# Kernel optimization log

Hardware: AMD Instinct MI355X
Metric: run time of the kernel (lower is better)

Reference implementation:

```python
import jax, jax.numpy as jnp
import numpy as np

N_USER, N_ITEM, D = 50000, 30000, 64
N = N_USER + N_ITEM
NNZ_UI, NNZ_R, NNZ_II = 1000000, 800000, 300000
IMG_F, TXT_F = 512, 384
EPS = 1e-5


def spmm(rows, cols, vals, x, n_out):
    # sparse [n_out, n_in] @ dense [n_in, d] via gather + segment-sum
    return jax.ops.segment_sum(vals[:, None] * x[cols], rows, num_segments=n_out)


def leaky_relu(x):
    return jnp.where(x >= 0, x, 0.01 * x)


def setup_inputs() -> dict:
    key = jax.random.key(0)
    ks = jax.random.split(key, 32)
    f = lambda i, shape, s=0.05: (jax.random.normal(ks[i], shape, dtype=jnp.float32) * s)
    inp = {
        'user_emb': f(0, (N_USER, D)),
        'item_emb': f(1, (N_ITEM, D)),
        'image_embedding': f(2, (N_ITEM, IMG_F), 1.0),
        'text_embedding': f(3, (N_ITEM, TXT_F), 1.0),
        'W_img': f(4, (IMG_F, D)), 'b_img': jnp.zeros((D,), jnp.float32),
        'bn_g_img': jnp.ones((D,), jnp.float32), 'bn_b_img': jnp.zeros((D,), jnp.float32),
        'W_txt': f(5, (TXT_F, D)), 'b_txt': jnp.zeros((D,), jnp.float32),
        'bn_g_txt': jnp.ones((D,), jnp.float32), 'bn_b_txt': jnp.zeros((D,), jnp.float32),
        'W_gate_img': f(6, (D, D)), 'b_gate_img': jnp.zeros((D,), jnp.float32),
        'W_gate_txt': f(7, (D, D)), 'b_gate_txt': jnp.zeros((D,), jnp.float32),
        'W_common1': f(8, (D, D)), 'b_common1': jnp.zeros((D,), jnp.float32),
        'w_common2': f(9, (D,)),
        'ui_vals': jax.random.uniform(ks[10], (NNZ_UI,), dtype=jnp.float32),
        'R_vals': jax.random.uniform(ks[11], (NNZ_R,), dtype=jnp.float32),
        'ii_img_vals': jax.random.uniform(ks[12], (NNZ_II,), dtype=jnp.float32),
        'ii_txt_vals': jax.random.uniform(ks[13], (NNZ_II,), dtype=jnp.float32),
        'ui_rows': jax.random.randint(ks[14], (NNZ_UI,), 0, N, dtype=jnp.int32),
        'ui_cols': jax.random.randint(ks[15], (NNZ_UI,), 0, N, dtype=jnp.int32),
        'R_rows': jax.random.randint(ks[16], (NNZ_R,), 0, N_USER, dtype=jnp.int32),
        'R_cols': jax.random.randint(ks[17], (NNZ_R,), 0, N_ITEM, dtype=jnp.int32),
        'ii_img_rows': jax.random.randint(ks[18], (NNZ_II,), 0, N_ITEM, dtype=jnp.int32),
        'ii_img_cols': jax.random.randint(ks[19], (NNZ_II,), 0, N_ITEM, dtype=jnp.int32),
        'ii_txt_rows': jax.random.randint(ks[20], (NNZ_II,), 0, N_ITEM, dtype=jnp.int32),
        'ii_txt_cols': jax.random.randint(ks[21], (NNZ_II,), 0, N_ITEM, dtype=jnp.int32),
    }
    return inp


def reference(user_emb, item_emb, image_embedding, text_embedding,
              W_img, b_img, bn_g_img, bn_b_img,
              W_txt, b_txt, bn_g_txt, bn_b_txt,
              W_gate_img, b_gate_img, W_gate_txt, b_gate_txt,
              W_common1, b_common1, w_common2,
              ui_vals, R_vals, ii_img_vals, ii_txt_vals,
              ui_rows, ui_cols, R_rows, R_cols,
              ii_img_rows, ii_img_cols, ii_txt_rows, ii_txt_cols):
    # ---- user_item_GCN: adj = original + diffusion (fused edge list) ----
    cat = jnp.concatenate([item_emb, user_emb], axis=0)  # [N, D], item first per source
    embs = [cat]
    for _ in range(2):
        cat = spmm(ui_rows, ui_cols, ui_vals, cat, N)
        embs.append(cat)
    content_embedding = jnp.stack(embs, axis=1).mean(axis=1)  # [N, D]

    # ---- modal projections (BN inference, dropout=eval identity) ----
    def project(x, W, b, g, beta):
        h = x @ W + b
        h = h * (g / jnp.sqrt(1.0 + EPS)) + beta  # BatchNorm1d, running stats (0, 1)
        return leaky_relu(h)

    img_feat = project(image_embedding, W_img, b_img, bn_g_img, bn_b_img)  # [I, D]
    txt_feat = project(text_embedding, W_txt, b_txt, bn_g_txt, bn_b_txt)

    # ---- item_item_GCN ----
    def modal_branch(feat, Wg, bg, rows, cols, vals):
        it = item_emb * jax.nn.sigmoid(feat @ Wg + bg)  # gated item embedding
        for _ in range(2):
            it = spmm(rows, cols, vals, it, N_ITEM)
        us = spmm(R_rows, R_cols, R_vals, it, N_USER)  # R @ item -> user
        return jnp.concatenate([us, it], axis=0)  # [N, D], user first per source

    image_ui = modal_branch(img_feat, W_gate_img, b_gate_img, ii_img_rows, ii_img_cols, ii_img_vals)
    text_ui = modal_branch(txt_feat, W_gate_txt, b_gate_txt, ii_txt_rows, ii_txt_cols, ii_txt_vals)

    # ---- gate_attention_fusion (non-tiktok: 2 modalities) ----
    def att_score(e):
        return leaky_relu(e @ W_common1 + b_common1) @ w_common2  # [N]

    att = jnp.stack([att_score(image_ui), att_score(text_ui)], axis=-1)  # [N, 2]
    w = jax.nn.softmax(att, axis=-1)
    common = w[:, 0:1] * image_ui + w[:, 1:2] * text_ui
    special_img = image_ui - common
    special_txt = text_ui - common

    return jnp.stack([content_embedding, special_img, special_txt, common], axis=0)  # [4, N, D]
```

## Files before the change

### kernel.cpp

```cpp
#include <hip/hip_runtime.h>

#define N_USER 50000
#define N_ITEM 30000
#define DIM    64
#define NTOT   80000
#define NNZ_UI 1000000
#define NNZ_R  800000
#define NNZ_II 300000
#define IMG_F  512
#define TXT_F  384

#define NROWS_ALL 190000
#define NNZ_ALL   2400000
#define BASE_R    NTOT
#define BASE_II   (NTOT + N_USER)
#define BASE_IT   (NTOT + N_USER + N_ITEM)

#define RB_BITS   9
#define RB_ROWS   512
#define NBUCK     ((NROWS_ALL + RB_ROWS - 1) / RB_ROWS)
#define NBLK_A2   400
#define EDG_A2    6000

__device__ __forceinline__ int edge_row(int i,
        const int* __restrict__ r0, const int* __restrict__ r1,
        const int* __restrict__ r2, const int* __restrict__ r3){
    if (i < NNZ_UI)                       return r0[i];
    if (i < NNZ_UI + NNZ_R)               return BASE_R  + r1[i - NNZ_UI];
    if (i < NNZ_UI + NNZ_R + NNZ_II)      return BASE_II + r2[i - NNZ_UI - NNZ_R];
    return BASE_IT + r3[i - NNZ_UI - NNZ_R - NNZ_II];
}

__device__ __forceinline__ void edge_all(int i,
        const int* __restrict__ r0, const int* __restrict__ c0, const float* __restrict__ v0,
        const int* __restrict__ r1, const int* __restrict__ c1, const float* __restrict__ v1,
        const int* __restrict__ r2, const int* __restrict__ c2, const float* __restrict__ v2,
        const int* __restrict__ r3, const int* __restrict__ c3, const float* __restrict__ v3,
        int& gr, int& col, float& val){
    if (i < NNZ_UI){
        gr = r0[i]; col = c0[i]; val = v0[i];
    } else if (i < NNZ_UI + NNZ_R){
        int j = i - NNZ_UI;               gr = BASE_R  + r1[j]; col = c1[j]; val = v1[j];
    } else if (i < NNZ_UI + NNZ_R + NNZ_II){
        int j = i - NNZ_UI - NNZ_R;       gr = BASE_II + r2[j]; col = c2[j]; val = v2[j];
    } else {
        int j = i - NNZ_UI - NNZ_R - NNZ_II; gr = BASE_IT + r3[j]; col = c3[j]; val = v3[j];
    }
}

__global__ __launch_bounds__(256) void k_bhist(const int* __restrict__ r0,
        const int* __restrict__ r1, const int* __restrict__ r2,
        const int* __restrict__ r3, int* __restrict__ bcnt){
    __shared__ int h[NBUCK];
    for (int i = threadIdx.x; i < NBUCK; i += 256) h[i] = 0;
    __syncthreads();
    const int stride = gridDim.x * 256;
    for (int i = blockIdx.x * 256 + threadIdx.x; i < NNZ_ALL; i += stride){
        int gr = edge_row(i, r0, r1, r2, r3);
        atomicAdd(&h[gr >> RB_BITS], 1);
    }
    __syncthreads();
    for (int i = threadIdx.x; i < NBUCK; i += 256){
        int c = h[i];
        if (c) atomicAdd(&bcnt[i], c);
    }
}

__global__ __launch_bounds__(512) void k_bscan(const int* __restrict__ bcnt,
        int* __restrict__ bbase, int* __restrict__ off){
    __shared__ int sh[512];
    const int t = threadIdx.x;
    int v = (t < NBUCK) ? bcnt[t] : 0;
    sh[t] = v;
    __syncthreads();
    for (int d = 1; d < 512; d <<= 1){
        int u = (t >= d) ? sh[t - d] : 0;
        __syncthreads();
        sh[t] += u;
        __syncthreads();
    }
    if (t < NBUCK) bbase[t] = sh[t] - v;
    if (t == NBUCK - 1){
        bbase[NBUCK] = sh[t];
        off[NROWS_ALL] = sh[t];
    }
}

__global__ __launch_bounds__(256) void k_bin(
        const int* __restrict__ r0, const int* __restrict__ c0, const float* __restrict__ v0,
        const int* __restrict__ r1, const int* __restrict__ c1, const float* __restrict__ v1,
        const int* __restrict__ r2, const int* __restrict__ c2, const float* __restrict__ v2,
        const int* __restrict__ r3, const int* __restrict__ c3, const float* __restrict__ v3,
        const int* __restrict__ bbase, int* __restrict__ bcur,
        int2* __restrict__ binned){
    __shared__ int lofs[NBUCK];
    __shared__ int lcur[NBUCK];
    const int t = threadIdx.x;
    for (int i = t; i < NBUCK; i += 256){ lofs[i] = 0; lcur[i] = 0; }
    __syncthreads();
    const int s0 = blockIdx.x * EDG_A2, s1 = s0 + EDG_A2;
    for (int i = s0 + t; i < s1; i += 256){
        int gr = edge_row(i, r0, r1, r2, r3);
        atomicAdd(&lofs[gr >> RB_BITS], 1);
    }
    __syncthreads();
    for (int i = t; i < NBUCK; i += 256){
        int c = lofs[i];
        lofs[i] = c ? (bbase[i] + atomicAdd(&bcur[i], c)) : 0;
    }
    __syncthreads();
    for (int i = s0 + t; i < s1; i += 256){
        int gr, col; float val;
        edge_all(i, r0, c0, v0, r1, c1, v1, r2, c2, v2, r3, c3, v3, gr, col, val);
        int b = gr >> RB_BITS;
        int slot = atomicAdd(&lcur[b], 1);
        binned[lofs[b] + slot] = make_int2((col << RB_BITS) | (gr & (RB_ROWS - 1)),
                                           __float_as_int(val));
    }
}

__global__ __launch_bounds__(256) void k_scatter(const int* __restrict__ bbase,
        const int2* __restrict__ binned, int* __restrict__ off,
        int2* __restrict__ csr){
    __shared__ int h[RB_ROWS];
    const int t = threadIdx.x;
    const int b = blockIdx.x;
    const int base = bbase[b];
    const int nb = bbase[b + 1] - base;
    h[t] = 0; h[t + 256] = 0;
    __syncthreads();
    for (int i = t; i < nb; i += 256)
        atomicAdd(&h[binned[base + i].x & (RB_ROWS - 1)], 1);
    __syncthreads();
    if (t < 64){
        int v[8], s = 0;
#pragma unroll
        for (int k = 0; k < 8; ++k){ v[k] = h[t * 8 + k]; s += v[k]; }
        int incl = s;
#pragma unroll
        for (int d = 1; d < 64; d <<= 1){
            int u = __shfl_up(incl, d, 64);
            if (t >= d) incl += u;
        }
        int run = incl - s;
#pragma unroll
        for (int k = 0; k < 8; ++k){ int tmp = v[k]; h[t * 8 + k] = run; run += tmp; }
    }
    __syncthreads();
    const int row0 = b << RB_BITS;
    for (int i = t; i < RB_ROWS; i += 256){
        int r = row0 + i;
        if (r < NROWS_ALL) off[r] = base + h[i];
    }
    __syncthreads();
    for (int i = t; i < nb; i += 256){
        int2 rec = binned[base + i];
        int lr = rec.x & (RB_ROWS - 1);
        int slot = atomicAdd(&h[lr], 1);
        csr[base + slot] = make_int2(rec.x >> RB_BITS, rec.y);
    }
}

__global__ void k_cat0(const float* __restrict__ item, const float* __restrict__ user,
                       float* __restrict__ o1){
    int i = blockIdx.x * 256 + threadIdx.x;
    const int ITEMS = N_ITEM * DIM;
    o1[i] = (i < ITEMS) ? item[i] : user[i - ITEMS];
}

__global__ void k_pull(const int* __restrict__ off, const int2* __restrict__ csr,
                       const float* __restrict__ x, float* __restrict__ y, int nrows){
    int t = blockIdx.x * 256 + threadIdx.x;
    int r = t >> 4;
    if (r >= nrows) return;
    int l = (t & 15) << 2;
    int s = off[r], e = off[r + 1];
    float4 a0 = {0.f, 0.f, 0.f, 0.f};
    float4 a1 = {0.f, 0.f, 0.f, 0.f};
    int j = s;
    for (; j + 2 <= e; j += 2){
        int2 e0 = csr[j];
        int2 e1 = csr[j + 1];
        float v0 = __int_as_float(e0.y);
        float v1 = __int_as_float(e1.y);
        const float4 x0 = *reinterpret_cast<const float4*>(x + ((long)e0.x << 6) + l);
        const float4 x1 = *reinterpret_cast<const float4*>(x + ((long)e1.x << 6) + l);
        a0.x = fmaf(v0, x0.x, a0.x);
        a0.y = fmaf(v0, x0.y, a0.y);
        a0.z = fmaf(v0, x0.z, a0.z);
        a0.w = fmaf(v0, x0.w, a0.w);
        a1.x = fmaf(v1, x1.x, a1.x);
        a1.y = fmaf(v1, x1.y, a1.y);
        a1.z = fmaf(v1, x1.z, a1.z);
        a1.w = fmaf(v1, x1.w, a1.w);
    }
    if (j < e){
        int2 e0 = csr[j];
        float v0 = __int_as_float(e0.y);
        const float4 x0 = *reinterpret_cast<const float4*>(x + ((long)e0.x << 6) + l);
        a0.x = fmaf(v0, x0.x, a0.x);
        a0.y = fmaf(v0, x0.y, a0.y);
        a0.z = fmaf(v0, x0.z, a0.z);
        a0.w = fmaf(v0, x0.w, a0.w);
    }
    a0.x += a1.x; a0.y += a1.y; a0.z += a1.z; a0.w += a1.w;
    *reinterpret_cast<float4*>(y + ((long)r << 6) + l) = a0;
}

__global__ void k_pull_mean(const int* __restrict__ off, const int2* __restrict__ csr,
                            const float* __restrict__ x, const float* __restrict__ a,
                            float* __restrict__ o0, int nrows){
    int t = blockIdx.x * 256 + threadIdx.x;
    int r = t >> 4;
    if (r >= nrows) return;
    int l = (t & 15) << 2;
    int s = off[r], e = off[r + 1];
    float4 a0 = {0.f, 0.f, 0.f, 0.f};
    float4 a1 = {0.f, 0.f, 0.f, 0.f};
    int j = s;
    for (; j + 2 <= e; j += 2){
        int2 e0 = csr[j];
        int2 e1 = csr[j + 1];
        float v0 = __int_as_float(e0.y);
        float v1 = __int_as_float(e1.y);
        const float4 x0 = *reinterpret_cast<const float4*>(x + ((long)e0.x << 6) + l);
        const float4 x1 = *reinterpret_cast<const float4*>(x + ((long)e1.x << 6) + l);
        a0.x = fmaf(v0, x0.x, a0.x);
        a0.y = fmaf(v0, x0.y, a0.y);
        a0.z = fmaf(v0, x0.z, a0.z);
        a0.w = fmaf(v0, x0.w, a0.w);
        a1.x = fmaf(v1, x1.x, a1.x);
        a1.y = fmaf(v1, x1.y, a1.y);
        a1.z = fmaf(v1, x1.z, a1.z);
        a1.w = fmaf(v1, x1.w, a1.w);
    }
    if (j < e){
        int2 e0 = csr[j];
        float v0 = __int_as_float(e0.y);
        const float4 x0 = *reinterpret_cast<const float4*>(x + ((long)e0.x << 6) + l);
        a0.x = fmaf(v0, x0.x, a0.x);
        a0.y = fmaf(v0, x0.y, a0.y);
        a0.z = fmaf(v0, x0.z, a0.z);
        a0.w = fmaf(v0, x0.w, a0.w);
    }
    const float4 av = *reinterpret_cast<const float4*>(a + ((long)r << 6) + l);
    const float4 xv = *reinterpret_cast<const float4*>(x + ((long)r << 6) + l);
    float4 o;
    o.x = (av.x + xv.x + a0.x + a1.x) * (1.0f / 3.0f);
    o.y = (av.y + xv.y + a0.y + a1.y) * (1.0f / 3.0f);
    o.z = (av.z + xv.z + a0.z + a1.z) * (1.0f / 3.0f);
    o.w = (av.w + xv.w + a0.w + a1.w) * (1.0f / 3.0f);
    *reinterpret_cast<float4*>(o0 + ((long)r << 6) + l) = o;
}

template<int K>
__global__ __launch_bounds__(256) void k_projgate(
        const float* __restrict__ X,
        const float* __restrict__ W,  const float* __restrict__ b,
        const float* __restrict__ g,  const float* __restrict__ beta,
        const float* __restrict__ Wg, const float* __restrict__ bg,
        const float* __restrict__ item, float* __restrict__ outP){
    __shared__ float xs[48][68];
    __shared__ float ws[64][64];
    const int t  = threadIdx.x;
    const int tr = t >> 4;
    const int tc = t & 15;
    const int row0 = blockIdx.x * 48;

    float acc[3][4];
#pragma unroll
    for (int i = 0; i < 3; ++i)
#pragma unroll
        for (int j = 0; j < 4; ++j) acc[i][j] = 0.f;

    for (int ks = 0; ks < K; ks += 64){
        __syncthreads();
#pragma unroll
        for (int i = 0; i < 3; ++i){
            int r = tr + 16 * i;
            *reinterpret_cast<float4*>(&xs[r][tc * 4]) =
                *reinterpret_cast<const float4*>(X + (long)(row0 + r) * K + ks + tc * 4);
        }
        {
            const float4* wsrc = reinterpret_cast<const float4*>(W + (long)ks * 64);
            float4* wdst = reinterpret_cast<float4*>(&ws[0][0]);
#pragma unroll
            for (int i = 0; i < 4; ++i) wdst[t + 256 * i] = wsrc[t + 256 * i];
        }
        __syncthreads();
#pragma unroll 8
        for (int kk = 0; kk < 64; kk += 2){
            float2 a[3];
#pragma unroll
            for (int i = 0; i < 3; ++i)
                a[i] = *reinterpret_cast<const float2*>(&xs[tr + 16 * i][kk]);
            float4 b0 = *reinterpret_cast<const float4*>(&ws[kk][tc * 4]);
            float4 b1 = *reinterpret_cast<const float4*>(&ws[kk + 1][tc * 4]);
#pragma unroll
            for (int i = 0; i < 3; ++i){
                acc[i][0] = fmaf(a[i].x, b0.x, acc[i][0]);
                acc[i][1] = fmaf(a[i].x, b0.y, acc[i][1]);
                acc[i][2] = fmaf(a[i].x, b0.z, acc[i][2]);
                acc[i][3] = fmaf(a[i].x, b0.w, acc[i][3]);
                acc[i][0] = fmaf(a[i].y, b1.x, acc[i][0]);
                acc[i][1] = fmaf(a[i].y, b1.y, acc[i][1]);
                acc[i][2] = fmaf(a[i].y, b1.z, acc[i][2]);
                acc[i][3] = fmaf(a[i].y, b1.w, acc[i][3]);
            }
        }
    }

    const float4 b4  = reinterpret_cast<const float4*>(b)[tc];
    const float4 g4  = reinterpret_cast<const float4*>(g)[tc];
    const float4 be4 = reinterpret_cast<const float4*>(beta)[tc];
    __syncthreads();
#pragma unroll
    for (int i = 0; i < 3; ++i){
        int r = tr + 16 * i;
        float4 h;
        h.x = (acc[i][0] + b4.x) * (g4.x * 0.99999500003749943f) + be4.x;
        h.y = (acc[i][1] + b4.y) * (g4.y * 0.99999500003749943f) + be4.y;
        h.z = (acc[i][2] + b4.z) * (g4.z * 0.99999500003749943f) + be4.z;
        h.w = (acc[i][3] + b4.w) * (g4.w * 0.99999500003749943f) + be4.w;
        h.x = (h.x >= 0.f) ? h.x : 0.01f * h.x;
        h.y = (h.y >= 0.f) ? h.y : 0.01f * h.y;
        h.z = (h.z >= 0.f) ? h.z : 0.01f * h.z;
        h.w = (h.w >= 0.f) ? h.w : 0.01f * h.w;
        *reinterpret_cast<float4*>(&xs[r][tc * 4]) = h;
    }
    {
        const float4* wsrc = reinterpret_cast<const float4*>(Wg);
        float4* wdst = reinterpret_cast<float4*>(&ws[0][0]);
#pragma unroll
        for (int i = 0; i < 4; ++i) wdst[t + 256 * i] = wsrc[t + 256 * i];
    }
    __syncthreads();

    float ac2[3][4];
#pragma unroll
    for (int i = 0; i < 3; ++i)
#pragma unroll
        for (int j = 0; j < 4; ++j) ac2[i][j] = 0.f;
#pragma unroll 8
    for (int kk = 0; kk < 64; kk += 2){
        float2 a[3];
#pragma unroll
        for (int i = 0; i < 3; ++i)
            a[i] = *reinterpret_cast<const float2*>(&xs[tr + 16 * i][kk]);
        float4 b0 = *reinterpret_cast<const float4*>(&ws[kk][tc * 4]);
        float4 b1 = *reinterpret_cast<const float4*>(&ws[kk + 1][tc * 4]);
#pragma unroll
        for (int i = 0; i < 3; ++i){
            ac2[i][0] = fmaf(a[i].x, b0.x, ac2[i][0]);
            ac2[i][1] = fmaf(a[i].x, b0.y, ac2[i][1]);
            ac2[i][2] = fmaf(a[i].x, b0.z, ac2[i][2]);
            ac2[i][3] = fmaf(a[i].x, b0.w, ac2[i][3]);
            ac2[i][0] = fmaf(a[i].y, b1.x, ac2[i][0]);
            ac2[i][1] = fmaf(a[i].y, b1.y, ac2[i][1]);
            ac2[i][2] = fmaf(a[i].y, b1.z, ac2[i][2]);
            ac2[i][3] = fmaf(a[i].y, b1.w, ac2[i][3]);
        }
    }

    const float4 bg4 = reinterpret_cast<const float4*>(bg)[tc];
#pragma unroll
    for (int i = 0; i < 3; ++i){
        int r = tr + 16 * i;
        const float4 iv = *reinterpret_cast<const float4*>(
                item + (long)(row0 + r) * 64 + tc * 4);
        float4 o;
        o.x = iv.x / (1.f + __expf(-(ac2[i][0] + bg4.x)));
        o.y = iv.y / (1.f + __expf(-(ac2[i][1] + bg4.y)));
        o.z = iv.z / (1.f + __expf(-(ac2[i][2] + bg4.z)));
        o.w = iv.w / (1.f + __expf(-(ac2[i][3] + bg4.w)));
        *reinterpret_cast<float4*>(outP + (long)(row0 + r) * 64 + tc * 4) = o;
    }
}

__global__ __launch_bounds__(256) void k_fuse(const float* __restrict__ img,
        const float* __restrict__ txt, const float* __restrict__ W1,
        const float* __restrict__ b1, const float* __restrict__ w2,
        float* __restrict__ out){
    __shared__ float si[64][68];
    __shared__ float st[64][68];
    __shared__ float w1s[64][64];
    const int t  = threadIdx.x;
    const int tr = t >> 4;
    const int tc = t & 15;
    const long row0 = (long)blockIdx.x * 64;

#pragma unroll
    for (int i = 0; i < 4; ++i){
        int r = tr + 16 * i;
        *reinterpret_cast<float4*>(&si[r][tc * 4]) =
            *reinterpret_cast<const float4*>(img + (row0 + r) * 64 + tc * 4);
        *reinterpret_cast<float4*>(&st[r][tc * 4]) =
            *reinterpret_cast<const float4*>(txt + (row0 + r) * 64 + tc * 4);
    }
    {
        const float4* wsrc = reinterpret_cast<const float4*>(W1);
        float4* wdst = reinterpret_cast<float4*>(&w1s[0][0]);
#pragma unroll
        for (int i = 0; i < 4; ++i) wdst[t + 256 * i] = wsrc[t + 256 * i];
    }
    __syncthreads();

    float ai[4][4], at[4][4];
#pragma unroll
    for (int i = 0; i < 4; ++i)
#pragma unroll
        for (int j = 0; j < 4; ++j){ ai[i][j] = 0.f; at[i][j] = 0.f; }

#pragma unroll 8
    for (int kk = 0; kk < 64; kk += 2){
        float4 b0 = *reinterpret_cast<const float4*>(&w1s[kk][tc * 4]);
        float4 b1v = *reinterpret_cast<const float4*>(&w1s[kk + 1][tc * 4]);
#pragma unroll
        for (int i = 0; i < 4; ++i){
            float2 a = *reinterpret_cast<const float2*>(&si[tr + 16 * i][kk]);
            float2 c = *reinterpret_cast<const float2*>(&st[tr + 16 * i][kk]);
            ai[i][0] = fmaf(a.x, b0.x, ai[i][0]);
            ai[i][1] = fmaf(a.x, b0.y, ai[i][1]);
            ai[i][2] = fmaf(a.x, b0.z, ai[i][2]);
            ai[i][3] = fmaf(a.x, b0.w, ai[i][3]);
            ai[i][0] = fmaf(a.y, b1v.x, ai[i][0]);
            ai[i][1] = fmaf(a.y, b1v.y, ai[i][1]);
            ai[i][2] = fmaf(a.y, b1v.z, ai[i][2]);
            ai[i][3] = fmaf(a.y, b1v.w, ai[i][3]);
            at[i][0] = fmaf(c.x, b0.x, at[i][0]);
            at[i][1] = fmaf(c.x, b0.y, at[i][1]);
            at[i][2] = fmaf(c.x, b0.z, at[i][2]);
            at[i][3] = fmaf(c.x, b0.w, at[i][3]);
            at[i][0] = fmaf(c.y, b1v.x, at[i][0]);
            at[i][1] = fmaf(c.y, b1v.y, at[i][1]);
            at[i][2] = fmaf(c.y, b1v.z, at[i][2]);
            at[i][3] = fmaf(c.y, b1v.w, at[i][3]);
        }
    }

    const float4 b14 = reinterpret_cast<const float4*>(b1)[tc];
    const float4 w24 = reinterpret_cast<const float4*>(w2)[tc];
    float pi[4], pt[4];
#pragma unroll
    for (int i = 0; i < 4; ++i){
        float hi0 = ai[i][0] + b14.x; hi0 = (hi0 >= 0.f) ? hi0 : 0.01f * hi0;
        float hi1 = ai[i][1] + b14.y; hi1 = (hi1 >= 0.f) ? hi1 : 0.01f * hi1;
        float hi2 = ai[i][2] + b14.z; hi2 = (hi2 >= 0.f) ? hi2 : 0.01f * hi2;
        float hi3 = ai[i][3] + b14.w; hi3 = (hi3 >= 0.f) ? hi3 : 0.01f * hi3;
        float ht0 = at[i][0] + b14.x; ht0 = (ht0 >= 0.f) ? ht0 : 0.01f * ht0;
        float ht1 = at[i][1] + b14.y; ht1 = (ht1 >= 0.f) ? ht1 : 0.01f * ht1;
        float ht2 = at[i][2] + b14.z; ht2 = (ht2 >= 0.f) ? ht2 : 0.01f * ht2;
        float ht3 = at[i][3] + b14.w; ht3 = (ht3 >= 0.f) ? ht3 : 0.01f * ht3;
        pi[i] = fmaf(hi0, w24.x, fmaf(hi1, w24.y, fmaf(hi2, w24.z, hi3 * w24.w)));
        pt[i] = fmaf(ht0, w24.x, fmaf(ht1, w24.y, fmaf(ht2, w24.z, ht3 * w24.w)));
    }
#pragma unroll
    for (int m = 1; m < 16; m <<= 1){
#pragma unroll
        for (int i = 0; i < 4; ++i){
            pi[i] += __shfl_xor(pi[i], m, 64);
            pt[i] += __shfl_xor(pt[i], m, 64);
        }
    }

    const long NTD = (long)NTOT * DIM;
#pragma unroll
    for (int i = 0; i < 4; ++i){
        int r = tr + 16 * i;
        float mx = fmaxf(pi[i], pt[i]);
        float ei = __expf(pi[i] - mx), et = __expf(pt[i] - mx);
        float inv = 1.f / (ei + et);
        float wi = ei * inv, wt = et * inv;
        const float4 ie = *reinterpret_cast<const float4*>(&si[r][tc * 4]);
        const float4 te = *reinterpret_cast<const float4*>(&st[r][tc * 4]);
        float4 cm, oi, ot;
        cm.x = wi * ie.x + wt * te.x;
        cm.y = wi * ie.y + wt * te.y;
        cm.z = wi * ie.z + wt * te.z;
        cm.w = wi * ie.w + wt * te.w;
        oi.x = ie.x - cm.x; oi.y = ie.y - cm.y; oi.z = ie.z - cm.z; oi.w = ie.w - cm.w;
        ot.x = te.x - cm.x; ot.y = te.y - cm.y; ot.z = te.z - cm.z; ot.w = te.w - cm.w;
        long o = (row0 + r) * 64 + tc * 4;
        *reinterpret_cast<float4*>(out + NTD + o)     = oi;
        *reinterpret_cast<float4*>(out + 2 * NTD + o) = ot;
        *reinterpret_cast<float4*>(out + 3 * NTD + o) = cm;
    }
}

extern "C" void kernel_launch(void* const* d_in, const int* in_sizes, int n_in,
                              void* d_out, int out_size, void* d_ws, size_t ws_size,
                              hipStream_t stream){
    const float* user_emb  = (const float*)d_in[0];
    const float* item_emb  = (const float*)d_in[1];
    const float* image_emb = (const float*)d_in[2];
    const float* text_emb  = (const float*)d_in[3];
    const float* W_img = (const float*)d_in[4];
    const float* b_img = (const float*)d_in[5];
    const float* g_img = (const float*)d_in[6];
    const float* be_img= (const float*)d_in[7];
    const float* W_txt = (const float*)d_in[8];
    const float* b_txt = (const float*)d_in[9];
    const float* g_txt = (const float*)d_in[10];
    const float* be_txt= (const float*)d_in[11];
    const float* W_gi  = (const float*)d_in[12];
    const float* b_gi  = (const float*)d_in[13];
    const float* W_gt  = (const float*)d_in[14];
    const float* b_gt  = (const float*)d_in[15];
    const float* W_c1  = (const float*)d_in[16];
    const float* b_c1  = (const float*)d_in[17];
    const float* w_c2  = (const float*)d_in[18];
    const float* ui_vals = (const float*)d_in[19];
    const float* R_vals  = (const float*)d_in[20];
    const float* ii_iv   = (const float*)d_in[21];
    const float* ii_tv   = (const float*)d_in[22];
    const int* ui_rows = (const int*)d_in[23];
    const int* ui_cols = (const int*)d_in[24];
    const int* R_rows  = (const int*)d_in[25];
    const int* R_cols  = (const int*)d_in[26];
    const int* ii_ir   = (const int*)d_in[27];
    const int* ii_ic   = (const int*)d_in[28];
    const int* ii_tr   = (const int*)d_in[29];
    const int* ii_tc   = (const int*)d_in[30];

    const long ND = (long)NTOT * DIM;
    const long ID = (long)N_ITEM * DIM;
    const long UD = (long)N_USER * DIM;

    float* out = (float*)d_out;
    float* o0 = out;
    float* o1 = out + ND;
    float* o2 = out + 2 * ND;
    float* o3 = out + 3 * ND;

    float* P = o3;
    float* Q = o3 + ID;

    int2* binned = (int2*)o0;

    int2* csr   = (int2*)d_ws;
    int*  off   = (int*)(csr + NNZ_ALL);
    int*  bcnt  = off + NROWS_ALL + 4;
    int*  bcur  = bcnt + NBUCK;
    int*  bbase = bcur + NBUCK;

    hipMemsetAsync(bcnt, 0, 2 * NBUCK * sizeof(int), stream);
    k_bhist<<<512, 256, 0, stream>>>(ui_rows, R_rows, ii_ir, ii_tr, bcnt);
    k_bscan<<<1, 512, 0, stream>>>(bcnt, bbase, off);
    k_bin<<<NBLK_A2, 256, 0, stream>>>(
        ui_rows, ui_cols, ui_vals,  R_rows, R_cols, R_vals,
        ii_ir, ii_ic, ii_iv,        ii_tr, ii_tc, ii_tv,
        bbase, bcur, binned);
    k_scatter<<<NBUCK, 256, 0, stream>>>(bbase, binned, off, csr);

    const int* offUI = off;
    const int* offR  = off + BASE_R;
    const int* offI2 = off + BASE_II;
    const int* offT2 = off + BASE_IT;

    k_cat0<<<ND / 256, 256, 0, stream>>>(item_emb, user_emb, o1);
    k_pull<<<NTOT / 16, 256, 0, stream>>>(offUI, csr, o1, o2, NTOT);
    k_pull_mean<<<NTOT / 16, 256, 0, stream>>>(offUI, csr, o2, o1, o0, NTOT);

    k_projgate<IMG_F><<<N_ITEM / 48, 256, 0, stream>>>(
        image_emb, W_img, b_img, g_img, be_img, W_gi, b_gi, item_emb, P);
    k_pull<<<N_ITEM / 16, 256, 0, stream>>>(offI2, csr, P, Q, N_ITEM);
    k_pull<<<N_ITEM / 16, 256, 0, stream>>>(offI2, csr, Q, o1 + UD, N_ITEM);
    k_pull<<<N_USER / 16, 256, 0, stream>>>(offR, csr, o1 + UD, o1, N_USER);

    k_projgate<TXT_F><<<N_ITEM / 48, 256, 0, stream>>>(
        text_emb, W_txt, b_txt, g_txt, be_txt, W_gt, b_gt, item_emb, P);
    k_pull<<<N_ITEM / 16, 256, 0, stream>>>(offT2, csr, P, Q, N_ITEM);
    k_pull<<<N_ITEM / 16, 256, 0, stream>>>(offT2, csr, Q, o2 + UD, N_ITEM);
    k_pull<<<N_USER / 16, 256, 0, stream>>>(offR, csr, o2 + UD, o2, N_USER);

    k_fuse<<<NTOT / 64, 256, 0, stream>>>(o1, o2, W_c1, b_c1, w_c2, out);
}
```

Before: 592.5 us.

## Batch image and text branches into joint launches and double-buffer projection GEMM

The image and text modal branches now share launches. One projection-plus-gate kernel covers both modalities by block index, and a two-way pull kernel runs each SpMM step for both branches at once. This roughly halves the branch launches and gives each launch twice as many independent blocks to fill the GPU. The projection GEMM also prefetches the next K chunk into registers while computing on a double-buffered shared tile, and reads four K values per LDS load. The cost is doubled shared memory per block, which may lower occupancy, and intermediate buffers reassigned into output slices o1 and o2 that must not overlap.

```diff
diff --git a/kernel.cpp b/kernel.cpp
--- a/kernel.cpp
+++ b/kernel.cpp
@@ -21,6 +21,10 @@
 #define NBUCK     ((NROWS_ALL + RB_ROWS - 1) / RB_ROWS)
 #define NBLK_A2   400
 #define EDG_A2    6000
+
+#define NBLK_PG   625
+#define NBLK_I16  1875
+#define NBLK_U16  3125
 
 __device__ __forceinline__ int edge_row(int i,
         const int* __restrict__ r0, const int* __restrict__ r1,
@@ -168,12 +172,9 @@
     o1[i] = (i < ITEMS) ? item[i] : user[i - ITEMS];
 }
 
-__global__ void k_pull(const int* __restrict__ off, const int2* __restrict__ csr,
-                       const float* __restrict__ x, float* __restrict__ y, int nrows){
-    int t = blockIdx.x * 256 + threadIdx.x;
-    int r = t >> 4;
-    if (r >= nrows) return;
-    int l = (t & 15) << 2;
+__device__ __forceinline__ void pull_body(const int* __restrict__ off,
+        const int2* __restrict__ csr, const float* __restrict__ x,
+        float* __restrict__ y, int r, int l){
     int s = off[r], e = off[r + 1];
     float4 a0 = {0.f, 0.f, 0.f, 0.f};
     float4 a1 = {0.f, 0.f, 0.f, 0.f};
@@ -205,6 +206,28 @@
     }
     a0.x += a1.x; a0.y += a1.y; a0.z += a1.z; a0.w += a1.w;
     *reinterpret_cast<float4*>(y + ((long)r << 6) + l) = a0;
+}
+
+__global__ void k_pull(const int* __restrict__ off, const int2* __restrict__ csr,
+                       const float* __restrict__ x, float* __restrict__ y, int nrows){
+    int t = blockIdx.x * 256 + threadIdx.x;
+    int r = t >> 4;
+    if (r >= nrows) return;
+    pull_body(off, csr, x, y, r, (t & 15) << 2);
+}
+
+__global__ void k_pull2(const int* __restrict__ offA, const int2* __restrict__ csr,
+                        const float* __restrict__ xA, float* __restrict__ yA,
+                        const int* __restrict__ offB, const float* __restrict__ xB,
+                        float* __restrict__ yB, int nrows, int nblk_half){
+    int b = blockIdx.x;
+    const int* off; const float* x; float* y;
+    if (b < nblk_half){ off = offA; x = xA; y = yA; }
+    else              { b -= nblk_half; off = offB; x = xB; y = yB; }
+    int t = b * 256 + threadIdx.x;
+    int r = t >> 4;
+    if (r >= nrows) return;
+    pull_body(off, csr, x, y, r, (t & 15) << 2);
 }
 
 __global__ void k_pull_mean(const int* __restrict__ off, const int2* __restrict__ csr,
@@ -253,19 +276,56 @@
     *reinterpret_cast<float4*>(o0 + ((long)r << 6) + l) = o;
 }
 
-template<int K>
-__global__ __launch_bounds__(256) void k_projgate(
-        const float* __restrict__ X,
-        const float* __restrict__ W,  const float* __restrict__ b,
-        const float* __restrict__ g,  const float* __restrict__ beta,
-        const float* __restrict__ Wg, const float* __restrict__ bg,
-        const float* __restrict__ item, float* __restrict__ outP){
-    __shared__ float xs[48][68];
-    __shared__ float ws[64][64];
+__global__ __launch_bounds__(256) void k_projgate2(
+        const float* __restrict__ Xi, const float* __restrict__ Wi,
+        const float* __restrict__ bi, const float* __restrict__ gi,
+        const float* __restrict__ bei, const float* __restrict__ Wgi,
+        const float* __restrict__ bgi,
+        const float* __restrict__ Xt, const float* __restrict__ Wt,
+        const float* __restrict__ bt, const float* __restrict__ gt,
+        const float* __restrict__ bet, const float* __restrict__ Wgt,
+        const float* __restrict__ bgt,
+        const float* __restrict__ item,
+        float* __restrict__ Pi, float* __restrict__ Pt){
+    __shared__ float xs[2][48][68];
+    __shared__ float ws[2][64][64];
     const int t  = threadIdx.x;
     const int tr = t >> 4;
     const int tc = t & 15;
-    const int row0 = blockIdx.x * 48;
+
+    const bool isTxt = blockIdx.x >= NBLK_PG;
+    const int  blk   = isTxt ? (blockIdx.x - NBLK_PG) : blockIdx.x;
+    const int  K     = isTxt ? TXT_F : IMG_F;
+    const int  NC    = K >> 6;
+    const float* X   = isTxt ? Xt  : Xi;
+    const float* W   = isTxt ? Wt  : Wi;
+    const float* bb  = isTxt ? bt  : bi;
+    const float* gg  = isTxt ? gt  : gi;
+    const float* be  = isTxt ? bet : bei;
+    const float* Wg  = isTxt ? Wgt : Wgi;
+    const float* bg  = isTxt ? bgt : bgi;
+    float* outP      = isTxt ? Pt  : Pi;
+    const int row0   = blk * 48;
+
+    float4 px[3], pw[4];
+#pragma unroll
+    for (int i = 0; i < 3; ++i)
+        px[i] = *reinterpret_cast<const float4*>(
+                X + (long)(row0 + tr + 16 * i) * K + tc * 4);
+    {
+        const float4* wsrc = reinterpret_cast<const float4*>(W);
+#pragma unroll
+        for (int i = 0; i < 4; ++i) pw[i] = wsrc[t + 256 * i];
+    }
+#pragma unroll
+    for (int i = 0; i < 3; ++i)
+        *reinterpret_cast<float4*>(&xs[0][tr + 16 * i][tc * 4]) = px[i];
+    {
+        float4* wdst = reinterpret_cast<float4*>(&ws[0][0][0]);
+#pragma unroll
+        for (int i = 0; i < 4; ++i) wdst[t + 256 * i] = pw[i];
+    }
+    __syncthreads();
 
     float acc[3][4];
 #pragma unroll
@@ -273,47 +333,64 @@
 #pragma unroll
         for (int j = 0; j < 4; ++j) acc[i][j] = 0.f;
 
-    for (int ks = 0; ks < K; ks += 64){
-        __syncthreads();
-#pragma unroll
-        for (int i = 0; i < 3; ++i){
-            int r = tr + 16 * i;
-            *reinterpret_cast<float4*>(&xs[r][tc * 4]) =
-                *reinterpret_cast<const float4*>(X + (long)(row0 + r) * K + ks + tc * 4);
+    for (int c = 0; c < NC; ++c){
+        const int cur = c & 1;
+        const bool has_next = (c + 1 < NC);
+        if (has_next){
+#pragma unroll
+            for (int i = 0; i < 3; ++i)
+                px[i] = *reinterpret_cast<const float4*>(
+                        X + (long)(row0 + tr + 16 * i) * K + (c + 1) * 64 + tc * 4);
+            const float4* wsrc = reinterpret_cast<const float4*>(W + (long)(c + 1) * 64 * 64);
+#pragma unroll
+            for (int i = 0; i < 4; ++i) pw[i] = wsrc[t + 256 * i];
         }
-        {
-            const float4* wsrc = reinterpret_cast<const float4*>(W + (long)ks * 64);
-            float4* wdst = reinterpret_cast<float4*>(&ws[0][0]);
-#pragma unroll
-            for (int i = 0; i < 4; ++i) wdst[t + 256 * i] = wsrc[t + 256 * i];
-        }
-        __syncthreads();
-#pragma unroll 8
-        for (int kk = 0; kk < 64; kk += 2){
-            float2 a[3];
+#pragma unroll 4
+        for (int kk = 0; kk < 64; kk += 4){
+            float4 a[3];
 #pragma unroll
             for (int i = 0; i < 3; ++i)
-                a[i] = *reinterpret_cast<const float2*>(&xs[tr + 16 * i][kk]);
-            float4 b0 = *reinterpret_cast<const float4*>(&ws[kk][tc * 4]);
-            float4 b1 = *reinterpret_cast<const float4*>(&ws[kk + 1][tc * 4]);
+                a[i] = *reinterpret_cast<const float4*>(&xs[cur][tr + 16 * i][kk]);
+            float4 w0 = *reinterpret_cast<const float4*>(&ws[cur][kk][tc * 4]);
+            float4 w1 = *reinterpret_cast<const float4*>(&ws[cur][kk + 1][tc * 4]);
+            float4 w2 = *reinterpret_cast<const float4*>(&ws[cur][kk + 2][tc * 4]);
+            float4 w3 = *reinterpret_cast<const float4*>(&ws[cur][kk + 3][tc * 4]);
 #pragma unroll
             for (int i = 0; i < 3; ++i){
-                acc[i][0] = fmaf(a[i].x, b0.x, acc[i][0]);
-                acc[i][1] = fmaf(a[i].x, b0.y, acc[i][1]);
-                acc[i][2] = fmaf(a[i].x, b0.z, acc[i][2]);
-                acc[i][3] = fmaf(a[i].x, b0.w, acc[i][3]);
-                acc[i][0] = fmaf(a[i].y, b1.x, acc[i][0]);
-                acc[i][1] = fmaf(a[i].y, b1.y, acc[i][1]);
-                acc[i][2] = fmaf(a[i].y, b1.z, acc[i][2]);
-                acc[i][3] = fmaf(a[i].y, b1.w, acc[i][3]);
+                acc[i][0] = fmaf(a[i].x, w0.x, acc[i][0]);
+                acc[i][1] = fmaf(a[i].x, w0.y, acc[i][1]);
+                acc[i][2] = fmaf(a[i].x, w0.z, acc[i][2]);
+                acc[i][3] = fmaf(a[i].x, w0.w, acc[i][3]);
+                acc[i][0] = fmaf(a[i].y, w1.x, acc[i][0]);
+                acc[i][1] = fmaf(a[i].y, w1.y, acc[i][1]);
+                acc[i][2] = fmaf(a[i].y, w1.z, acc[i][2]);
+                acc[i][3] = fmaf(a[i].y, w1.w, acc[i][3]);
+                acc[i][0] = fmaf(a[i].z, w2.x, acc[i][0]);
+                acc[i][1] = fmaf(a[i].z, w2.y, acc[i][1]);
+                acc[i][2] = fmaf(a[i].z, w2.z, acc[i][2]);
+                acc[i][3] = fmaf(a[i].z, w2.w, acc[i][3]);
+                acc[i][0] = fmaf(a[i].w, w3.x, acc[i][0]);
+                acc[i][1] = fmaf(a[i].w, w3.y, acc[i][1]);
+                acc[i][2] = fmaf(a[i].w, w3.z, acc[i][2]);
+                acc[i][3] = fmaf(a[i].w, w3.w, acc[i][3]);
             }
         }
-    }
-
-    const float4 b4  = reinterpret_cast<const float4*>(b)[tc];
-    const float4 g4  = reinterpret_cast<const float4*>(g)[tc];
-    const float4 be4 = reinterpret_cast<const float4*>(beta)[tc];
-    __syncthreads();
+        if (has_next){
+            const int nxt = cur ^ 1;
+#pragma unroll
+            for (int i = 0; i < 3; ++i)
+                *reinterpret_cast<float4*>(&xs[nxt][tr + 16 * i][tc * 4]) = px[i];
+            float4* wdst = reinterpret_cast<float4*>(&ws[nxt][0][0]);
+#pragma unroll
+            for (int i = 0; i < 4; ++i) wdst[t + 256 * i] = pw[i];
+            __syncthreads();
+        }
+    }
+    __syncthreads();
+
+    const float4 b4  = reinterpret_cast<const float4*>(bb)[tc];
+    const float4 g4  = reinterpret_cast<const float4*>(gg)[tc];
+    const float4 be4 = reinterpret_cast<const float4*>(be)[tc];
 #pragma unroll
     for (int i = 0; i < 3; ++i){
         int r = tr + 16 * i;
@@ -326,39 +403,48 @@
         h.y = (h.y >= 0.f) ? h.y : 0.01f * h.y;
         h.z = (h.z >= 0.f) ? h.z : 0.01f * h.z;
         h.w = (h.w >= 0.f) ? h.w : 0.01f * h.w;
-        *reinterpret_cast<float4*>(&xs[r][tc * 4]) = h;
+        *reinterpret_cast<float4*>(&xs[0][r][tc * 4]) = h;
     }
     {
         const float4* wsrc = reinterpret_cast<const float4*>(Wg);
-        float4* wdst = reinterpret_cast<float4*>(&ws[0][0]);
+        float4* wdst = reinterpret_cast<float4*>(&ws[0][0][0]);
 #pragma unroll
         for (int i = 0; i < 4; ++i) wdst[t + 256 * i] = wsrc[t + 256 * i];
     }
     __syncthreads();
 
-    float ac2[3][4];
 #pragma unroll
     for (int i = 0; i < 3; ++i)
 #pragma unroll
-        for (int j = 0; j < 4; ++j) ac2[i][j] = 0.f;
-#pragma unroll 8
-    for (int kk = 0; kk < 64; kk += 2){
-        float2 a[3];
+        for (int j = 0; j < 4; ++j) acc[i][j] = 0.f;
+#pragma unroll 4
+    for (int kk = 0; kk < 64; kk += 4){
+        float4 a[3];
 #pragma unroll
         for (int i = 0; i < 3; ++i)
-            a[i] = *reinterpret_cast<const float2*>(&xs[tr + 16 * i][kk]);
-        float4 b0 = *reinterpret_cast<const float4*>(&ws[kk][tc * 4]);
-        float4 b1 = *reinterpret_cast<const float4*>(&ws[kk + 1][tc * 4]);
+            a[i] = *reinterpret_cast<const float4*>(&xs[0][tr + 16 * i][kk]);
+        float4 w0 = *reinterpret_cast<const float4*>(&ws[0][kk][tc * 4]);
+        float4 w1 = *reinterpret_cast<const float4*>(&ws[0][kk + 1][tc * 4]);
+        float4 w2 = *reinterpret_cast<const float4*>(&ws[0][kk + 2][tc * 4]);
+        float4 w3 = *reinterpret_cast<const float4*>(&ws[0][kk + 3][tc * 4]);
 #pragma unroll
         for (int i = 0; i < 3; ++i){
-            ac2[i][0] = fmaf(a[i].x, b0.x, ac2[i][0]);
-            ac2[i][1] = fmaf(a[i].x, b0.y, ac2[i][1]);
-            ac2[i][2] = fmaf(a[i].x, b0.z, ac2[i][2]);
-            ac2[i][3] = fmaf(a[i].x, b0.w, ac2[i][3]);
-            ac2[i][0] = fmaf(a[i].y, b1.x, ac2[i][0]);
-            ac2[i][1] = fmaf(a[i].y, b1.y, ac2[i][1]);
-            ac2[i][2] = fmaf(a[i].y, b1.z, ac2[i][2]);
-            ac2[i][3] = fmaf(a[i].y, b1.w, ac2[i][3]);
+            acc[i][0] = fmaf(a[i].x, w0.x, acc[i][0]);
+            acc[i][1] = fmaf(a[i].x, w0.y, acc[i][1]);
+            acc[i][2] = fmaf(a[i].x, w0.z, acc[i][2]);
+            acc[i][3] = fmaf(a[i].x, w0.w, acc[i][3]);
+            acc[i][0] = fmaf(a[i].y, w1.x, acc[i][0]);
+            acc[i][1] = fmaf(a[i].y, w1.y, acc[i][1]);
+            acc[i][2] = fmaf(a[i].y, w1.z, acc[i][2]);
+            acc[i][3] = fmaf(a[i].y, w1.w, acc[i][3]);
+            acc[i][0] = fmaf(a[i].z, w2.x, acc[i][0]);
+            acc[i][1] = fmaf(a[i].z, w2.y, acc[i][1]);
+            acc[i][2] = fmaf(a[i].z, w2.z, acc[i][2]);
+            acc[i][3] = fmaf(a[i].z, w2.w, acc[i][3]);
+            acc[i][0] = fmaf(a[i].w, w3.x, acc[i][0]);
+            acc[i][1] = fmaf(a[i].w, w3.y, acc[i][1]);
+            acc[i][2] = fmaf(a[i].w, w3.z, acc[i][2]);
+            acc[i][3] = fmaf(a[i].w, w3.w, acc[i][3]);
         }
     }
 
@@ -369,10 +455,10 @@
         const float4 iv = *reinterpret_cast<const float4*>(
                 item + (long)(row0 + r) * 64 + tc * 4);
         float4 o;
-        o.x = iv.x / (1.f + __expf(-(ac2[i][0] + bg4.x)));
-        o.y = iv.y / (1.f + __expf(-(ac2[i][1] + bg4.y)));
-        o.z = iv.z / (1.f + __expf(-(ac2[i][2] + bg4.z)));
-        o.w = iv.w / (1.f + __expf(-(ac2[i][3] + bg4.w)));
+        o.x = iv.x / (1.f + __expf(-(acc[i][0] + bg4.x)));
+        o.y = iv.y / (1.f + __expf(-(acc[i][1] + bg4.y)));
+        o.z = iv.z / (1.f + __expf(-(acc[i][2] + bg4.z)));
+        o.w = iv.w / (1.f + __expf(-(acc[i][3] + bg4.w)));
         *reinterpret_cast<float4*>(outP + (long)(row0 + r) * 64 + tc * 4) = o;
     }
 }
@@ -532,8 +618,10 @@
     float* o2 = out + 2 * ND;
     float* o3 = out + 3 * ND;
 
-    float* P = o3;
-    float* Q = o3 + ID;
+    float* P_img = o3;
+    float* P_txt = o3 + ID;
+    float* Q_img = o2;
+    float* Q_txt = o1;
 
     int2* binned = (int2*)o0;
 
@@ -561,17 +649,16 @@
     k_pull<<<NTOT / 16, 256, 0, stream>>>(offUI, csr, o1, o2, NTOT);
     k_pull_mean<<<NTOT / 16, 256, 0, stream>>>(offUI, csr, o2, o1, o0, NTOT);
 
-    k_projgate<IMG_F><<<N_ITEM / 48, 256, 0, stream>>>(
-        image_emb, W_img, b_img, g_img, be_img, W_gi, b_gi, item_emb, P);
-    k_pull<<<N_ITEM / 16, 256, 0, stream>>>(offI2, csr, P, Q, N_ITEM);
-    k_pull<<<N_ITEM / 16, 256, 0, stream>>>(offI2, csr, Q, o1 + UD, N_ITEM);
-    k_pull<<<N_USER / 16, 256, 0, stream>>>(offR, csr, o1 + UD, o1, N_USER);
-
-    k_projgate<TXT_F><<<N_ITEM / 48, 256, 0, stream>>>(
-        text_emb, W_txt, b_txt, g_txt, be_txt, W_gt, b_gt, item_emb, P);
-    k_pull<<<N_ITEM / 16, 256, 0, stream>>>(offT2, csr, P, Q, N_ITEM);
-    k_pull<<<N_ITEM / 16, 256, 0, stream>>>(offT2, csr, Q, o2 + UD, N_ITEM);
-    k_pull<<<N_USER / 16, 256, 0, stream>>>(offR, csr, o2 + UD, o2, N_USER);
+    k_projgate2<<<2 * NBLK_PG, 256, 0, stream>>>(
+        image_emb, W_img, b_img, g_img, be_img, W_gi, b_gi,
+        text_emb,  W_txt, b_txt, g_txt, be_txt, W_gt, b_gt,
+        item_emb, P_img, P_txt);
+    k_pull2<<<2 * NBLK_I16, 256, 0, stream>>>(
+        offI2, csr, P_img, Q_img, offT2, P_txt, Q_txt, N_ITEM, NBLK_I16);
+    k_pull2<<<2 * NBLK_I16, 256, 0, stream>>>(
+        offI2, csr, Q_img, o1 + UD, offT2, Q_txt, o2 + UD, N_ITEM, NBLK_I16);
+    k_pull2<<<2 * NBLK_U16, 256, 0, stream>>>(
+        offR, csr, o1 + UD, o1, offR, o2 + UD, o2, N_USER, NBLK_U16);
 
     k_fuse<<<NTOT / 64, 256, 0, stream>>>(o1, o2, W_c1, b_c1, w_c2, out);
 }
```

Result: slower. 615.7 us (+3.9%).
